# Optimization experiments

Hardware: AMD Instinct MI355X
Metric: run time of the kernel (lower is better)

## Reference

```python
import jax, jax.numpy as jnp
import numpy as np

BN_EPS = 1e-5
DIST_MIN = 1e-10


def _three_nn(p1t, p2t):
    # p1t: [B,N,3], p2t: [B,S,3] -> squared dists/idx of 3 nearest, [B,N,3]
    d2 = (jnp.sum(p1t * p1t, -1, keepdims=True)
          - 2.0 * jnp.einsum('bnc,bsc->bns', p1t, p2t)
          + jnp.sum(p2t * p2t, -1)[:, None, :])  # [B,N,S]
    neg, idx = jax.lax.top_k(-d2, 3)
    return -neg, idx


def _gather_knn(f2t, idx):
    # f2t: [B,S,D], idx: [B,N,3] -> [B,N,3,D]
    return jax.vmap(lambda f, i: f[i])(f2t, idx)


def _conv_bn_relu(x, W, b, g, beta):
    # x: [B,C,N]; 1x1 conv == channel GEMM, then train-mode BN, then ReLU
    y = jnp.einsum('oc,bcn->bon', W, x) + b[None, :, None]
    mean = jnp.mean(y, axis=(0, 2), keepdims=True)
    var = jnp.mean((y - mean) ** 2, axis=(0, 2), keepdims=True)
    yn = (y - mean) * jax.lax.rsqrt(var + BN_EPS)
    return jax.nn.relu(yn * g[None, :, None] + beta[None, :, None])


def setup_inputs() -> dict:
    key = jax.random.key(0)
    ks = jax.random.split(key, 10)
    B, N, S, D1, D2 = 4, 8192, 2048, 128, 256
    C_in, C_mid, C_out = D1 + D2, 256, 256
    inp = {
        'pos1': jax.random.normal(ks[0], (B, 3, N), jnp.float32),
        'pos2': jax.random.normal(ks[1], (B, 3, S), jnp.float32),
        'feature1': jax.random.normal(ks[2], (B, D1, N), jnp.float32),
        'feature2': jax.random.normal(ks[3], (B, D2, S), jnp.float32),
        'W1': jax.random.normal(ks[4], (C_mid, C_in), jnp.float32) / np.sqrt(C_in),
        'b1': jnp.zeros((C_mid,), jnp.float32),
        'g1': jnp.ones((C_mid,), jnp.float32),
        'beta1': jnp.zeros((C_mid,), jnp.float32),
        'W2': jax.random.normal(ks[5], (C_out, C_mid), jnp.float32) / np.sqrt(C_mid),
        'b2': jnp.zeros((C_out,), jnp.float32),
        'g2': jnp.ones((C_out,), jnp.float32),
        'beta2': jnp.zeros((C_out,), jnp.float32),
    }
    return inp


def reference(pos1, pos2, feature1, feature2, W1, b1, g1, beta1, W2, b2, g2, beta2):
    B = pos1.shape[0]
    p1t = jnp.transpose(pos1, (0, 2, 1))  # [B,N,3]
    p2t = jnp.transpose(pos2, (0, 2, 1))  # [B,S,3]
    dists, idx = _three_nn(p1t, p2t)      # [B,N,3]
    dists = jnp.maximum(dists, DIST_MIN)
    w = 1.0 / dists
    w = w / jnp.sum(w, -1, keepdims=True)  # [B,N,3]
    f2t = jnp.transpose(feature2, (0, 2, 1))  # [B,S,D2]
    gathered = _gather_knn(f2t, idx)           # [B,N,3,D2]
    interp = jnp.sum(gathered * w[..., None], axis=2)  # [B,N,D2]
    interp = jnp.transpose(interp, (0, 2, 1))          # [B,D2,N]
    feat = jnp.concatenate([interp, feature1], axis=1)  # [B,D2+D1,N]
    feat = _conv_bn_relu(feat, W1, b1, g1, beta1)
    feat = _conv_bn_relu(feat, W2, b2, g2, beta2)
    return feat
```

## Files before the change

### kernel.cpp

```cpp
#include <hip/hip_runtime.h>
#include <hip/hip_bf16.h>

constexpr int B = 4, N = 8192, S = 2048;

typedef __attribute__((ext_vector_type(8))) short short8;
typedef __attribute__((ext_vector_type(4))) float v4f;

__device__ inline float u2f(ushort u) {
    union { ushort u; __hip_bfloat16 h; } c; c.u = u; return __bfloat162float(c.h);
}
__device__ inline ushort f2u(float f) {
    union { ushort u; __hip_bfloat16 h; } c; c.h = __float2bfloat16(f); return c.u;
}
__device__ inline void async_lds16(const void* g, void* l) {
    __builtin_amdgcn_global_load_lds(
        (const __attribute__((address_space(1))) unsigned*)g,
        (__attribute__((address_space(3))) unsigned*)l, 16, 0, 0);
}
__device__ inline short8 ld8(const ushort* p) { return *(const short8*)p; }

__global__ __launch_bounds__(256) void prep_kernel(
    const float* __restrict__ W1, const float* __restrict__ W2,
    const float* __restrict__ pos2,
    __hip_bfloat16* __restrict__ W1r, __hip_bfloat16* __restrict__ W2r,
    float4* __restrict__ p2pack, float* __restrict__ zero_region)
{
    int i = blockIdx.x * 256 + threadIdx.x;
    if (i < 12288) {
        int kk = i >> 10, q = (i >> 8) & 3, o = i & 255;
        const float* src = W1 + o * 384 + kk * 32 + q * 8;
        float4 a = *(const float4*)src, b = *(const float4*)(src + 4);
        union { short8 s; ushort u[8]; } pk;
        pk.u[0] = f2u(a.x); pk.u[1] = f2u(a.y); pk.u[2] = f2u(a.z); pk.u[3] = f2u(a.w);
        pk.u[4] = f2u(b.x); pk.u[5] = f2u(b.y); pk.u[6] = f2u(b.z); pk.u[7] = f2u(b.w);
        *(short8*)((ushort*)W1r + i * 8) = pk.s;
    } else if (i < 20480) {
        int u = i - 12288;
        int kk = u >> 10, q = (u >> 8) & 3, o = u & 255;
        const float* src = W2 + o * 256 + kk * 32 + q * 8;
        float4 a = *(const float4*)src, b = *(const float4*)(src + 4);
        union { short8 s; ushort u[8]; } pk;
        pk.u[0] = f2u(a.x); pk.u[1] = f2u(a.y); pk.u[2] = f2u(a.z); pk.u[3] = f2u(a.w);
        pk.u[4] = f2u(b.x); pk.u[5] = f2u(b.y); pk.u[6] = f2u(b.z); pk.u[7] = f2u(b.w);
        *(short8*)((ushort*)W2r + u * 8) = pk.s;
    } else if (i < 21504) {
        zero_region[i - 20480] = 0.f;
    } else if (i < 21504 + B * S) {
        int u = i - 21504;
        int b = u >> 11, s = u & (S - 1);
        float x = pos2[(b * 3 + 0) * S + s];
        float y = pos2[(b * 3 + 1) * S + s];
        float z = pos2[(b * 3 + 2) * S + s];
        p2pack[u] = make_float4(x, y, z, x * x + y * y + z * z);
    }
}

__global__ __launch_bounds__(512) void knn_kernel(
    const float* __restrict__ pos1, const float4* __restrict__ p2pack,
    float* __restrict__ wgt, int* __restrict__ idxb)
{
    __shared__ float dLs[8][64][3];
    __shared__ int   iLs[8][64][3];
    const int b = blockIdx.y;
    const int t = threadIdx.x;
    const int lane = t & 63;
    const int w = __builtin_amdgcn_readfirstlane(t >> 6);
    const int qi = blockIdx.x * 64 + lane;

    const float x1 = pos1[(b * 3 + 0) * N + qi];
    const float y1 = pos1[(b * 3 + 1) * N + qi];
    const float z1 = pos1[(b * 3 + 2) * N + qi];
    const float t1 = x1 * x1 + y1 * y1 + z1 * z1;

    const float4* __restrict__ pp = p2pack + b * S + w * 256;

    float d0 = 3.4e38f, d1 = 3.4e38f, d2 = 3.4e38f;
    int i0 = 0x7fffffff, i1 = 0x7fffffff, i2 = 0x7fffffff;

    #pragma unroll 8
    for (int i = 0; i < 256; ++i) {
        float4 p = pp[i];
        float dot = fmaf(x1, p.x, fmaf(y1, p.y, z1 * p.z));
        float dd = fmaf(-2.f, dot, t1) + p.w;
        int s = w * 256 + i;
        bool c0 = dd < d0, c1 = dd < d1, c2 = dd < d2;
        i2 = c1 ? i1 : (c2 ? s : i2);
        i1 = c0 ? i0 : (c1 ? s : i1);
        i0 = c0 ? s : i0;
        float nd1 = __builtin_amdgcn_fmed3f(dd, d0, d1);
        float nd2 = __builtin_amdgcn_fmed3f(dd, d1, d2);
        d0 = fminf(d0, dd);
        d1 = nd1; d2 = nd2;
    }

    dLs[w][lane][0] = d0; dLs[w][lane][1] = d1; dLs[w][lane][2] = d2;
    iLs[w][lane][0] = i0; iLs[w][lane][1] = i1; iLs[w][lane][2] = i2;
    __syncthreads();

    if (t < 64) {
        float f0 = dLs[0][t][0], f1 = dLs[0][t][1], f2 = dLs[0][t][2];
        int   j0 = iLs[0][t][0], j1 = iLs[0][t][1], j2 = iLs[0][t][2];
        #pragma unroll
        for (int c = 1; c < 8; ++c) {
            #pragma unroll
            for (int k = 0; k < 3; ++k) {
                float d = dLs[c][t][k]; int id = iLs[c][t][k];
                bool l0 = (d < f0) || (d == f0 && id < j0);
                bool l1 = (d < f1) || (d == f1 && id < j1);
                bool l2 = (d < f2) || (d == f2 && id < j2);
                if (l0)      { f2 = f1; j2 = j1; f1 = f0; j1 = j0; f0 = d; j0 = id; }
                else if (l1) { f2 = f1; j2 = j1; f1 = d; j1 = id; }
                else if (l2) { f2 = d; j2 = id; }
            }
        }
        float w0 = 1.f / fmaxf(f0, 1e-10f);
        float w1 = 1.f / fmaxf(f1, 1e-10f);
        float w2 = 1.f / fmaxf(f2, 1e-10f);
        float inv = 1.f / (w0 + w1 + w2);
        j0 = ((unsigned)j0 < S) ? j0 : 0;
        j1 = ((unsigned)j1 < S) ? j1 : 0;
        j2 = ((unsigned)j2 < S) ? j2 : 0;
        int base = (b * N + blockIdx.x * 64 + t) * 3;
        wgt[base + 0] = w0 * inv; wgt[base + 1] = w1 * inv; wgt[base + 2] = w2 * inv;
        idxb[base + 0] = j0; idxb[base + 1] = j1; idxb[base + 2] = j2;
    }
}

__global__ __launch_bounds__(256) void transpose_k(
    const float* __restrict__ in, __hip_bfloat16* __restrict__ out,
    int L, int C)
{
    __shared__ ushort tl[64][66];
    const int b = blockIdx.z;
    const int l0 = blockIdx.x * 64, c0 = blockIdx.y * 64;
    const int t = threadIdx.x;
    const float* ip = in + (size_t)b * C * L;
    const int lr = t & 63, cb = t >> 6;
    #pragma unroll
    for (int i = 0; i < 16; ++i) {
        int c = cb + 4 * i;
        tl[lr][c] = f2u(ip[(size_t)(c0 + c) * L + l0 + lr]);
    }
    __syncthreads();
    ushort* op = (ushort*)out + (size_t)b * L * C;
    const int cp = t & 31, lrow = t >> 5;
    #pragma unroll
    for (int i = 0; i < 8; ++i) {
        int l = lrow + 8 * i;
        ushort2 v;
        v.x = tl[l][2 * cp];
        v.y = tl[l][2 * cp + 1];
        *(ushort2*)(op + (size_t)(l0 + l) * C + c0 + 2 * cp) = v;
    }
}

__global__ __launch_bounds__(256) void gemm1_kernel(
    const __hip_bfloat16* __restrict__ Wr, const float* __restrict__ bias,
    const __hip_bfloat16* __restrict__ f2T, const __hip_bfloat16* __restrict__ f1T,
    const int* __restrict__ idxb, const float* __restrict__ wgt,
    __hip_bfloat16* __restrict__ y, float* __restrict__ sums)
{
    __shared__ __align__(16) ushort Xs[64 * 384];
    __shared__ __align__(16) ushort Wbuf[2 * 8192];
    const int t = threadIdx.x;
    const int b = blockIdx.y;
    const int n0 = blockIdx.x * 64;
    const int w = t >> 6, lane = t & 63;
    const int q = lane >> 4, r = lane & 15, r7 = r & 7;

    {
        const char* g0 = (const char*)Wr;
        #pragma unroll
        for (int jj = 0; jj < 4; ++jj)
            async_lds16(g0 + jj * 4096 + t * 16,
                        (char*)Wbuf + jj * 4096 + w * 1024);
    }

    {
        const int lp = t & 31, ro = t >> 5;
        #pragma unroll
        for (int it = 0; it < 8; ++it) {
            int rr = ro + 8 * it;
            int base = (b * N + n0 + rr) * 3;
            int s0 = idxb[base], s1 = idxb[base + 1], s2 = idxb[base + 2];
            s0 = ((unsigned)s0 < S) ? s0 : 0;
            s1 = ((unsigned)s1 < S) ? s1 : 0;
            s2 = ((unsigned)s2 < S) ? s2 : 0;
            float w0 = wgt[base], w1 = wgt[base + 1], w2 = wgt[base + 2];
            union { short8 s; ushort u[8]; } a, c, d, o;
            a.s = ld8((const ushort*)f2T + ((size_t)b * S + s0) * 256 + 8 * lp);
            c.s = ld8((const ushort*)f2T + ((size_t)b * S + s1) * 256 + 8 * lp);
            d.s = ld8((const ushort*)f2T + ((size_t)b * S + s2) * 256 + 8 * lp);
            #pragma unroll
            for (int j = 0; j < 8; ++j)
                o.u[j] = f2u(w0 * u2f(a.u[j]) + w1 * u2f(c.u[j]) + w2 * u2f(d.u[j]));
            *(short8*)(Xs + rr * 384 + ((lp ^ ro) * 8)) = o.s;
        }
    }
    {
        const int lp = t & 15, ro = t >> 4;
        #pragma unroll
        for (int it = 0; it < 4; ++it) {
            int rr = ro + 16 * it;
            short8 v = ld8((const ushort*)f1T + ((size_t)b * N + n0 + rr) * 128 + 8 * lp);
            int c = 32 + lp;
            *(short8*)(Xs + rr * 384 + ((c ^ (rr & 7)) * 8)) = v;
        }
    }
    __syncthreads();

    v4f acc[4][4];
    #pragma unroll
    for (int mt = 0; mt < 4; ++mt)
        #pragma unroll
        for (int nf = 0; nf < 4; ++nf) acc[mt][nf] = (v4f){0.f, 0.f, 0.f, 0.f};

    for (int kk = 0; kk < 12; ++kk) {
        if (kk < 11) {
            const char* g = (const char*)Wr + (kk + 1) * 16384;
            char* l = (char*)Wbuf + ((kk + 1) & 1) * 16384;
            #pragma unroll
            for (int jj = 0; jj < 4; ++jj)
                async_lds16(g + jj * 4096 + t * 16, l + jj * 4096 + w * 1024);
        }
        const ushort* Wb = Wbuf + (kk & 1) * 8192;
        short8 af[4], bf[4];
        #pragma unroll
        for (int mt = 0; mt < 4; ++mt)
            af[mt] = ld8(Wb + q * 2048 + (w * 64 + mt * 16 + r) * 8);
        #pragma unroll
        for (int nf = 0; nf < 4; ++nf)
            bf[nf] = ld8(Xs + (nf * 16 + r) * 384 + (((kk * 4 + q) ^ r7) * 8));
        #pragma unroll
        for (int mt = 0; mt < 4; ++mt)
            #pragma unroll
            for (int nf = 0; nf < 4; ++nf)
                acc[mt][nf] = __builtin_amdgcn_mfma_f32_16x16x32_bf16(
                    af[mt], bf[nf], acc[mt][nf], 0, 0, 0);
        __syncthreads();
    }

    float* statS = (float*)Xs;
    float* statQ = statS + 256;
    #pragma unroll
    for (int mt = 0; mt < 4; ++mt) {
        int ob = w * 64 + mt * 16 + q * 4;
        float4 bi = *(const float4*)(bias + ob);
        float sj0 = 0, sj1 = 0, sj2 = 0, sj3 = 0;
        float qj0 = 0, qj1 = 0, qj2 = 0, qj3 = 0;
        #pragma unroll
        for (int nf = 0; nf < 4; ++nf) {
            int n = n0 + nf * 16 + r;
            float v0 = acc[mt][nf][0] + bi.x, v1 = acc[mt][nf][1] + bi.y;
            float v2 = acc[mt][nf][2] + bi.z, v3 = acc[mt][nf][3] + bi.w;
            ushort4 pk; pk.x = f2u(v0); pk.y = f2u(v1); pk.z = f2u(v2); pk.w = f2u(v3);
            *(ushort4*)((ushort*)y + ((size_t)b * N + n) * 256 + ob) = pk;
            sj0 += v0; sj1 += v1; sj2 += v2; sj3 += v3;
            qj0 += v0 * v0; qj1 += v1 * v1; qj2 += v2 * v2; qj3 += v3 * v3;
        }
        #pragma unroll
        for (int m = 1; m <= 8; m <<= 1) {
            sj0 += __shfl_xor(sj0, m); sj1 += __shfl_xor(sj1, m);
            sj2 += __shfl_xor(sj2, m); sj3 += __shfl_xor(sj3, m);
            qj0 += __shfl_xor(qj0, m); qj1 += __shfl_xor(qj1, m);
            qj2 += __shfl_xor(qj2, m); qj3 += __shfl_xor(qj3, m);
        }
        if (r == 0) {
            statS[ob + 0] = sj0; statS[ob + 1] = sj1;
            statS[ob + 2] = sj2; statS[ob + 3] = sj3;
            statQ[ob + 0] = qj0; statQ[ob + 1] = qj1;
            statQ[ob + 2] = qj2; statQ[ob + 3] = qj3;
        }
    }
    __syncthreads();
    atomicAdd(&sums[t], statS[t]);
    atomicAdd(&sums[256 + t], statQ[t]);
}

__global__ __launch_bounds__(256) void gemm2_kernel(
    const __hip_bfloat16* __restrict__ Wr, const float* __restrict__ bias,
    const float* __restrict__ sums1, const float* __restrict__ g1,
    const float* __restrict__ be1,
    __hip_bfloat16* __restrict__ y, float* __restrict__ sums)
{
    __shared__ __align__(16) ushort Xs[64 * 256];
    __shared__ __align__(16) ushort Wbuf[2 * 8192];
    __shared__ float ssA[256], ssB[256];
    const int t = threadIdx.x;
    const int b = blockIdx.y;
    const int n0 = blockIdx.x * 64;
    const int w = t >> 6, lane = t & 63;
    const int q = lane >> 4, r = lane & 15, r7 = r & 7;

    {
        const char* g0 = (const char*)Wr;
        #pragma unroll
        for (int jj = 0; jj < 4; ++jj)
            async_lds16(g0 + jj * 4096 + t * 16,
                        (char*)Wbuf + jj * 4096 + w * 1024);
    }

    {
        float sv = sums1[t], qv = sums1[256 + t];
        float mean = sv * (1.f / 32768.f);
        float var = qv * (1.f / 32768.f) - mean * mean;
        float rstd = rsqrtf(var + 1e-5f);
        float sc = g1[t] * rstd;
        ssA[t] = sc;
        ssB[t] = be1[t] - mean * sc;
    }
    __syncthreads();

    {
        const int lp = t & 31, ro = t >> 5;
        #pragma unroll
        for (int it = 0; it < 8; ++it) {
            int rr = ro + 8 * it;
            union { short8 s; ushort u[8]; } v, o;
            v.s = ld8((const ushort*)y + ((size_t)b * N + n0 + rr) * 256 + 8 * lp);
            #pragma unroll
            for (int j = 0; j < 8; ++j)
                o.u[j] = f2u(fmaxf(u2f(v.u[j]) * ssA[8 * lp + j] + ssB[8 * lp + j], 0.f));
            *(short8*)(Xs + rr * 256 + ((lp ^ ro) * 8)) = o.s;
        }
    }
    __syncthreads();

    v4f acc[4][4];
    #pragma unroll
    for (int mt = 0; mt < 4; ++mt)
        #pragma unroll
        for (int nf = 0; nf < 4; ++nf) acc[mt][nf] = (v4f){0.f, 0.f, 0.f, 0.f};

    for (int kk = 0; kk < 8; ++kk) {
        if (kk < 7) {
            const char* g = (const char*)Wr + (kk + 1) * 16384;
            char* l = (char*)Wbuf + ((kk + 1) & 1) * 16384;
            #pragma unroll
            for (int jj = 0; jj < 4; ++jj)
                async_lds16(g + jj * 4096 + t * 16, l + jj * 4096 + w * 1024);
        }
        const ushort* Wb = Wbuf + (kk & 1) * 8192;
        short8 af[4], bf[4];
        #pragma unroll
        for (int mt = 0; mt < 4; ++mt)
            af[mt] = ld8(Wb + q * 2048 + (w * 64 + mt * 16 + r) * 8);
        #pragma unroll
        for (int nf = 0; nf < 4; ++nf)
            bf[nf] = ld8(Xs + (nf * 16 + r) * 256 + (((kk * 4 + q) ^ r7) * 8));
        #pragma unroll
        for (int mt = 0; mt < 4; ++mt)
            #pragma unroll
            for (int nf = 0; nf < 4; ++nf)
                acc[mt][nf] = __builtin_amdgcn_mfma_f32_16x16x32_bf16(
                    af[mt], bf[nf], acc[mt][nf], 0, 0, 0);
        __syncthreads();
    }

    float* statS = (float*)Xs;
    float* statQ = statS + 256;
    #pragma unroll
    for (int mt = 0; mt < 4; ++mt) {
        int ob = w * 64 + mt * 16 + q * 4;
        float4 bi = *(const float4*)(bias + ob);
        float sj0 = 0, sj1 = 0, sj2 = 0, sj3 = 0;
        float qj0 = 0, qj1 = 0, qj2 = 0, qj3 = 0;
        #pragma unroll
        for (int nf = 0; nf < 4; ++nf) {
            int n = n0 + nf * 16 + r;
            float v0 = acc[mt][nf][0] + bi.x, v1 = acc[mt][nf][1] + bi.y;
            float v2 = acc[mt][nf][2] + bi.z, v3 = acc[mt][nf][3] + bi.w;
            ushort4 pk; pk.x = f2u(v0); pk.y = f2u(v1); pk.z = f2u(v2); pk.w = f2u(v3);
            *(ushort4*)((ushort*)y + ((size_t)b * N + n) * 256 + ob) = pk;
            sj0 += v0; sj1 += v1; sj2 += v2; sj3 += v3;
            qj0 += v0 * v0; qj1 += v1 * v1; qj2 += v2 * v2; qj3 += v3 * v3;
        }
        #pragma unroll
        for (int m = 1; m <= 8; m <<= 1) {
            sj0 += __shfl_xor(sj0, m); sj1 += __shfl_xor(sj1, m);
            sj2 += __shfl_xor(sj2, m); sj3 += __shfl_xor(sj3, m);
            qj0 += __shfl_xor(qj0, m); qj1 += __shfl_xor(qj1, m);
            qj2 += __shfl_xor(qj2, m); qj3 += __shfl_xor(qj3, m);
        }
        if (r == 0) {
            statS[ob + 0] = sj0; statS[ob + 1] = sj1;
            statS[ob + 2] = sj2; statS[ob + 3] = sj3;
            statQ[ob + 0] = qj0; statQ[ob + 1] = qj1;
            statQ[ob + 2] = qj2; statQ[ob + 3] = qj3;
        }
    }
    __syncthreads();
    atomicAdd(&sums[t], statS[t]);
    atomicAdd(&sums[256 + t], statQ[t]);
}

__global__ __launch_bounds__(256) void final_kernel(
    const __hip_bfloat16* __restrict__ Y, const float* __restrict__ sums2,
    const float* __restrict__ g2, const float* __restrict__ be2,
    float* __restrict__ out)
{
    __shared__ float tl[64][65];
    __shared__ float ssA[64], ssB[64];
    const int t = threadIdx.x;
    const int b = blockIdx.z;
    const int n0 = blockIdx.x * 64, c0 = blockIdx.y * 64;

    if (t < 64) {
        int c = c0 + t;
        float sv = sums2[c], qv = sums2[256 + c];
        float mean = sv * (1.f / 32768.f);
        float var = qv * (1.f / 32768.f) - mean * mean;
        float rstd = rsqrtf(var + 1e-5f);
        float sc = g2[c] * rstd;
        ssA[t] = sc;
        ssB[t] = be2[c] - mean * sc;
    }
    __syncthreads();

    const int nl = t >> 3, cho = 8 * (t & 7);
    #pragma unroll
    for (int it = 0; it < 2; ++it) {
        int n = nl + 32 * it;
        union { short8 s; ushort u[8]; } v;
        v.s = ld8((const ushort*)Y + ((size_t)b * N + n0 + n) * 256 + c0 + cho);
        #pragma unroll
        for (int j = 0; j < 8; ++j)
            tl[n][cho + j] = fmaxf(u2f(v.u[j]) * ssA[cho + j] + ssB[cho + j], 0.f);
    }
    __syncthreads();

    const int cl = t >> 4, n4 = (t & 15) * 4;
    #pragma unroll
    for (int it = 0; it < 4; ++it) {
        int c = cl + 16 * it;
        float4 v;
        v.x = tl[n4 + 0][c]; v.y = tl[n4 + 1][c];
        v.z = tl[n4 + 2][c]; v.w = tl[n4 + 3][c];
        *(float4*)(out + ((size_t)b * 256 + c0 + c) * N + n0 + n4) = v;
    }
}

extern "C" void kernel_launch(void* const* d_in, const int* in_sizes, int n_in,
                              void* d_out, int out_size, void* d_ws, size_t ws_size,
                              hipStream_t stream)
{
    (void)in_sizes; (void)n_in; (void)out_size;
    if (ws_size < (30u << 20)) return;

    const float* pos1 = (const float*)d_in[0];
    const float* pos2 = (const float*)d_in[1];
    const float* f1   = (const float*)d_in[2];
    const float* f2   = (const float*)d_in[3];
    const float* W1   = (const float*)d_in[4];
    const float* b1   = (const float*)d_in[5];
    const float* g1   = (const float*)d_in[6];
    const float* be1  = (const float*)d_in[7];
    const float* W2   = (const float*)d_in[8];
    const float* b2   = (const float*)d_in[9];
    const float* g2   = (const float*)d_in[10];
    const float* be2  = (const float*)d_in[11];

    char* ws = (char*)d_ws;
    int*   idxb  = (int*)(ws + 0);
    float* wgt   = (float*)(ws + 393216);
    float* sums1 = (float*)(ws + 786432);
    float* sums2 = sums1 + 512;
    __hip_bfloat16* W1r = (__hip_bfloat16*)(ws + 819200);
    __hip_bfloat16* W2r = (__hip_bfloat16*)(ws + 1015808);
    float4* p2pack = (float4*)(ws + 1310720);
    __hip_bfloat16* f2T = (__hip_bfloat16*)(ws + (2u << 20));
    __hip_bfloat16* f1T = (__hip_bfloat16*)(ws + (6u << 20));
    __hip_bfloat16* y   = (__hip_bfloat16*)(ws + (14u << 20));

    prep_kernel<<<116, 256, 0, stream>>>(W1, W2, pos2, W1r, W2r, p2pack, sums1);

    knn_kernel<<<dim3(N / 64, B), 512, 0, stream>>>(pos1, p2pack, wgt, idxb);

    transpose_k<<<dim3(S / 64, 256 / 64, B), 256, 0, stream>>>(f2, f2T, S, 256);
    transpose_k<<<dim3(N / 64, 128 / 64, B), 256, 0, stream>>>(f1, f1T, N, 128);

    gemm1_kernel<<<dim3(N / 64, B), 256, 0, stream>>>(
        W1r, b1, f2T, f1T, idxb, wgt, y, sums1);
    gemm2_kernel<<<dim3(N / 64, B), 256, 0, stream>>>(
        W2r, b2, sums1, g1, be1, y, sums2);
    final_kernel<<<dim3(N / 64, 256 / 64, B), 256, 0, stream>>>(
        y, sums2, g2, be2, (float*)d_out);
}
```

Measured before the change: 200.9 us.

## Fuse kNN into GEMM1 and merge prep with feature transposes

Measured after the change: 204.4 us. No clear change (+1.7%).

```diff
diff --git a/kernel.cpp b/kernel.cpp
--- a/kernel.cpp
+++ b/kernel.cpp
@@ -19,178 +19,174 @@
 }
 __device__ inline short8 ld8(const ushort* p) { return *(const short8*)p; }
 
-__global__ __launch_bounds__(256) void prep_kernel(
+__device__ inline void transpose_tile(
+    const float* __restrict__ ip, ushort* __restrict__ op,
+    int L, int C, int l0, int c0, int t, ushort (*tl)[66])
+{
+    const int lr = t & 63, cb = t >> 6;
+    #pragma unroll
+    for (int i = 0; i < 16; ++i) {
+        int c = cb + 4 * i;
+        tl[lr][c] = f2u(ip[(size_t)(c0 + c) * L + l0 + lr]);
+    }
+    __syncthreads();
+    const int cp = t & 31, lrow = t >> 5;
+    #pragma unroll
+    for (int i = 0; i < 8; ++i) {
+        int l = lrow + 8 * i;
+        ushort2 v;
+        v.x = tl[l][2 * cp]; v.y = tl[l][2 * cp + 1];
+        *(ushort2*)(op + (size_t)(l0 + l) * C + c0 + 2 * cp) = v;
+    }
+}
+
+__global__ __launch_bounds__(256) void prep_all(
     const float* __restrict__ W1, const float* __restrict__ W2,
-    const float* __restrict__ pos2,
-    __hip_bfloat16* __restrict__ W1r, __hip_bfloat16* __restrict__ W2r,
-    float4* __restrict__ p2pack, float* __restrict__ zero_region)
-{
-    int i = blockIdx.x * 256 + threadIdx.x;
-    if (i < 12288) {
-        int kk = i >> 10, q = (i >> 8) & 3, o = i & 255;
-        const float* src = W1 + o * 384 + kk * 32 + q * 8;
-        float4 a = *(const float4*)src, b = *(const float4*)(src + 4);
-        union { short8 s; ushort u[8]; } pk;
-        pk.u[0] = f2u(a.x); pk.u[1] = f2u(a.y); pk.u[2] = f2u(a.z); pk.u[3] = f2u(a.w);
-        pk.u[4] = f2u(b.x); pk.u[5] = f2u(b.y); pk.u[6] = f2u(b.z); pk.u[7] = f2u(b.w);
-        *(short8*)((ushort*)W1r + i * 8) = pk.s;
-    } else if (i < 20480) {
-        int u = i - 12288;
-        int kk = u >> 10, q = (u >> 8) & 3, o = u & 255;
-        const float* src = W2 + o * 256 + kk * 32 + q * 8;
-        float4 a = *(const float4*)src, b = *(const float4*)(src + 4);
-        union { short8 s; ushort u[8]; } pk;
-        pk.u[0] = f2u(a.x); pk.u[1] = f2u(a.y); pk.u[2] = f2u(a.z); pk.u[3] = f2u(a.w);
-        pk.u[4] = f2u(b.x); pk.u[5] = f2u(b.y); pk.u[6] = f2u(b.z); pk.u[7] = f2u(b.w);
-        *(short8*)((ushort*)W2r + u * 8) = pk.s;
-    } else if (i < 21504) {
-        zero_region[i - 20480] = 0.f;
-    } else if (i < 21504 + B * S) {
-        int u = i - 21504;
-        int b = u >> 11, s = u & (S - 1);
-        float x = pos2[(b * 3 + 0) * S + s];
-        float y = pos2[(b * 3 + 1) * S + s];
-        float z = pos2[(b * 3 + 2) * S + s];
-        p2pack[u] = make_float4(x, y, z, x * x + y * y + z * z);
-    }
-}
-
-__global__ __launch_bounds__(512) void knn_kernel(
+    const float* __restrict__ pos2, const float* __restrict__ f2,
+    const float* __restrict__ f1,
+    ushort* __restrict__ W1r, ushort* __restrict__ W2r,
+    float4* __restrict__ p2pack, float* __restrict__ zero_region,
+    ushort* __restrict__ f2T, ushort* __restrict__ f1T)
+{
+    __shared__ ushort tl[64][66];
+    const int bid = blockIdx.x;
+    const int t = threadIdx.x;
+    if (bid < 512) {
+        int b = bid >> 7, ct = (bid >> 5) & 3, st = bid & 31;
+        transpose_tile(f2 + (size_t)b * 256 * S, f2T + (size_t)b * S * 256,
+                       S, 256, st * 64, ct * 64, t, tl);
+    } else if (bid < 1536) {
+        int u = bid - 512;
+        int b = u >> 8, ct = (u >> 7) & 1, lt = u & 127;
+        transpose_tile(f1 + (size_t)b * 128 * N, f1T + (size_t)b * N * 128,
+                       N, 128, lt * 64, ct * 64, t, tl);
+    } else {
+        int i = (bid - 1536) * 256 + t;
+        if (i < 12288) {
+            int kk = i >> 10, qq = (i >> 8) & 3, o = i & 255;
+            const float* src = W1 + o * 384 + kk * 32 + qq * 8;
+            float4 a = *(const float4*)src, bb = *(const float4*)(src + 4);
+            union { short8 s; ushort u[8]; } pk;
+            pk.u[0]=f2u(a.x); pk.u[1]=f2u(a.y); pk.u[2]=f2u(a.z); pk.u[3]=f2u(a.w);
+            pk.u[4]=f2u(bb.x); pk.u[5]=f2u(bb.y); pk.u[6]=f2u(bb.z); pk.u[7]=f2u(bb.w);
+            *(short8*)(W1r + i * 8) = pk.s;
+        } else if (i < 20480) {
+            int u = i - 12288;
+            int kk = u >> 10, qq = (u >> 8) & 3, o = u & 255;
+            const float* src = W2 + o * 256 + kk * 32 + qq * 8;
+            float4 a = *(const float4*)src, bb = *(const float4*)(src + 4);
+            union { short8 s; ushort u[8]; } pk;
+            pk.u[0]=f2u(a.x); pk.u[1]=f2u(a.y); pk.u[2]=f2u(a.z); pk.u[3]=f2u(a.w);
+            pk.u[4]=f2u(bb.x); pk.u[5]=f2u(bb.y); pk.u[6]=f2u(bb.z); pk.u[7]=f2u(bb.w);
+            *(short8*)(W2r + u * 8) = pk.s;
+        } else if (i < 21504) {
+            zero_region[i - 20480] = 0.f;
+        } else if (i < 21504 + B * S) {
+            int u = i - 21504;
+            int b = u >> 11, s = u & (S - 1);
+            float x = pos2[(b * 3 + 0) * S + s];
+            float y = pos2[(b * 3 + 1) * S + s];
+            float z = pos2[(b * 3 + 2) * S + s];
+            p2pack[u] = make_float4(x, y, z, x * x + y * y + z * z);
+        }
+    }
+}
+
+__global__ __launch_bounds__(256) void knn_gemm1(
     const float* __restrict__ pos1, const float4* __restrict__ p2pack,
-    float* __restrict__ wgt, int* __restrict__ idxb)
-{
-    __shared__ float dLs[8][64][3];
-    __shared__ int   iLs[8][64][3];
-    const int b = blockIdx.y;
+    const ushort* __restrict__ W1r, const float* __restrict__ bias1,
+    const ushort* __restrict__ f2T, const ushort* __restrict__ f1T,
+    ushort* __restrict__ y, float* __restrict__ sums)
+{
+    __shared__ __align__(16) char smem[81920];
+    ushort* Xs   = (ushort*)smem;
+    ushort* Wbuf = (ushort*)(smem + 49152);
+    float*  dL   = (float*)(smem + 65536);
+    int*    iL   = (int*)  (smem + 65536 + 3072);
+    float*  wgtL = (float*)(smem + 65536 + 6144);
+    int*    idxL = (int*)  (smem + 65536 + 6912);
+
     const int t = threadIdx.x;
     const int lane = t & 63;
     const int w = __builtin_amdgcn_readfirstlane(t >> 6);
-    const int qi = blockIdx.x * 64 + lane;
-
-    const float x1 = pos1[(b * 3 + 0) * N + qi];
-    const float y1 = pos1[(b * 3 + 1) * N + qi];
-    const float z1 = pos1[(b * 3 + 2) * N + qi];
-    const float t1 = x1 * x1 + y1 * y1 + z1 * z1;
-
-    const float4* __restrict__ pp = p2pack + b * S + w * 256;
-
-    float d0 = 3.4e38f, d1 = 3.4e38f, d2 = 3.4e38f;
-    int i0 = 0x7fffffff, i1 = 0x7fffffff, i2 = 0x7fffffff;
-
-    #pragma unroll 8
-    for (int i = 0; i < 256; ++i) {
-        float4 p = pp[i];
-        float dot = fmaf(x1, p.x, fmaf(y1, p.y, z1 * p.z));
-        float dd = fmaf(-2.f, dot, t1) + p.w;
-        int s = w * 256 + i;
-        bool c0 = dd < d0, c1 = dd < d1, c2 = dd < d2;
-        i2 = c1 ? i1 : (c2 ? s : i2);
-        i1 = c0 ? i0 : (c1 ? s : i1);
-        i0 = c0 ? s : i0;
-        float nd1 = __builtin_amdgcn_fmed3f(dd, d0, d1);
-        float nd2 = __builtin_amdgcn_fmed3f(dd, d1, d2);
-        d0 = fminf(d0, dd);
-        d1 = nd1; d2 = nd2;
-    }
-
-    dLs[w][lane][0] = d0; dLs[w][lane][1] = d1; dLs[w][lane][2] = d2;
-    iLs[w][lane][0] = i0; iLs[w][lane][1] = i1; iLs[w][lane][2] = i2;
-    __syncthreads();
-
+    const int b = blockIdx.y;
+    const int n0 = blockIdx.x * 64;
+    const int q = lane >> 4, r = lane & 15, r7 = r & 7;
+
+    #pragma unroll
+    for (int jj = 0; jj < 4; ++jj)
+        async_lds16((const char*)W1r + jj * 4096 + t * 16,
+                    (char*)Wbuf + jj * 4096 + w * 1024);
+
+    {
+        const int qi = n0 + lane;
+        const float x1 = pos1[(b * 3 + 0) * N + qi];
+        const float y1 = pos1[(b * 3 + 1) * N + qi];
+        const float z1 = pos1[(b * 3 + 2) * N + qi];
+        const float t1 = x1 * x1 + y1 * y1 + z1 * z1;
+        const float4* __restrict__ pp = p2pack + b * S + w * 512;
+        float d0 = 3.4e38f, d1 = 3.4e38f, d2 = 3.4e38f;
+        int i0 = 0x7fffffff, i1 = 0x7fffffff, i2 = 0x7fffffff;
+        #pragma unroll 8
+        for (int i = 0; i < 512; ++i) {
+            float4 p = pp[i];
+            float dot = fmaf(x1, p.x, fmaf(y1, p.y, z1 * p.z));
+            float dd = fmaf(-2.f, dot, t1) + p.w;
+            int s = w * 512 + i;
+            bool c0 = dd < d0, c1 = dd < d1, c2 = dd < d2;
+            i2 = c1 ? i1 : (c2 ? s : i2);
+            i1 = c0 ? i0 : (c1 ? s : i1);
+            i0 = c0 ? s : i0;
+            float nd1 = __builtin_amdgcn_fmed3f(dd, d0, d1);
+            float nd2 = __builtin_amdgcn_fmed3f(dd, d1, d2);
+            d0 = fminf(d0, dd);
+            d1 = nd1; d2 = nd2;
+        }
+        int base = (w * 64 + lane) * 3;
+        dL[base + 0] = d0; dL[base + 1] = d1; dL[base + 2] = d2;
+        iL[base + 0] = i0; iL[base + 1] = i1; iL[base + 2] = i2;
+    }
+    __syncthreads();
     if (t < 64) {
-        float f0 = dLs[0][t][0], f1 = dLs[0][t][1], f2 = dLs[0][t][2];
-        int   j0 = iLs[0][t][0], j1 = iLs[0][t][1], j2 = iLs[0][t][2];
-        #pragma unroll
-        for (int c = 1; c < 8; ++c) {
+        float f0 = dL[t*3+0], fv1 = dL[t*3+1], fv2 = dL[t*3+2];
+        int   j0 = iL[t*3+0], j1 = iL[t*3+1], j2 = iL[t*3+2];
+        #pragma unroll
+        for (int c = 1; c < 4; ++c) {
+            int cb = (c * 64 + t) * 3;
             #pragma unroll
             for (int k = 0; k < 3; ++k) {
-                float d = dLs[c][t][k]; int id = iLs[c][t][k];
-                bool l0 = (d < f0) || (d == f0 && id < j0);
-                bool l1 = (d < f1) || (d == f1 && id < j1);
-                bool l2 = (d < f2) || (d == f2 && id < j2);
-                if (l0)      { f2 = f1; j2 = j1; f1 = f0; j1 = j0; f0 = d; j0 = id; }
-                else if (l1) { f2 = f1; j2 = j1; f1 = d; j1 = id; }
-                else if (l2) { f2 = d; j2 = id; }
+                float d = dL[cb + k]; int id = iL[cb + k];
+                bool l0 = (d < f0)  || (d == f0  && id < j0);
+                bool l1 = (d < fv1) || (d == fv1 && id < j1);
+                bool l2 = (d < fv2) || (d == fv2 && id < j2);
+                if (l0)      { fv2 = fv1; j2 = j1; fv1 = f0; j1 = j0; f0 = d; j0 = id; }
+                else if (l1) { fv2 = fv1; j2 = j1; fv1 = d; j1 = id; }
+                else if (l2) { fv2 = d; j2 = id; }
             }
         }
         float w0 = 1.f / fmaxf(f0, 1e-10f);
-        float w1 = 1.f / fmaxf(f1, 1e-10f);
-        float w2 = 1.f / fmaxf(f2, 1e-10f);
+        float w1 = 1.f / fmaxf(fv1, 1e-10f);
+        float w2 = 1.f / fmaxf(fv2, 1e-10f);
         float inv = 1.f / (w0 + w1 + w2);
         j0 = ((unsigned)j0 < S) ? j0 : 0;
         j1 = ((unsigned)j1 < S) ? j1 : 0;
         j2 = ((unsigned)j2 < S) ? j2 : 0;
-        int base = (b * N + blockIdx.x * 64 + t) * 3;
-        wgt[base + 0] = w0 * inv; wgt[base + 1] = w1 * inv; wgt[base + 2] = w2 * inv;
-        idxb[base + 0] = j0; idxb[base + 1] = j1; idxb[base + 2] = j2;
-    }
-}
-
-__global__ __launch_bounds__(256) void transpose_k(
-    const float* __restrict__ in, __hip_bfloat16* __restrict__ out,
-    int L, int C)
-{
-    __shared__ ushort tl[64][66];
-    const int b = blockIdx.z;
-    const int l0 = blockIdx.x * 64, c0 = blockIdx.y * 64;
-    const int t = threadIdx.x;
-    const float* ip = in + (size_t)b * C * L;
-    const int lr = t & 63, cb = t >> 6;
-    #pragma unroll
-    for (int i = 0; i < 16; ++i) {
-        int c = cb + 4 * i;
-        tl[lr][c] = f2u(ip[(size_t)(c0 + c) * L + l0 + lr]);
-    }
-    __syncthreads();
-    ushort* op = (ushort*)out + (size_t)b * L * C;
-    const int cp = t & 31, lrow = t >> 5;
-    #pragma unroll
-    for (int i = 0; i < 8; ++i) {
-        int l = lrow + 8 * i;
-        ushort2 v;
-        v.x = tl[l][2 * cp];
-        v.y = tl[l][2 * cp + 1];
-        *(ushort2*)(op + (size_t)(l0 + l) * C + c0 + 2 * cp) = v;
-    }
-}
-
-__global__ __launch_bounds__(256) void gemm1_kernel(
-    const __hip_bfloat16* __restrict__ Wr, const float* __restrict__ bias,
-    const __hip_bfloat16* __restrict__ f2T, const __hip_bfloat16* __restrict__ f1T,
-    const int* __restrict__ idxb, const float* __restrict__ wgt,
-    __hip_bfloat16* __restrict__ y, float* __restrict__ sums)
-{
-    __shared__ __align__(16) ushort Xs[64 * 384];
-    __shared__ __align__(16) ushort Wbuf[2 * 8192];
-    const int t = threadIdx.x;
-    const int b = blockIdx.y;
-    const int n0 = blockIdx.x * 64;
-    const int w = t >> 6, lane = t & 63;
-    const int q = lane >> 4, r = lane & 15, r7 = r & 7;
-
-    {
-        const char* g0 = (const char*)Wr;
-        #pragma unroll
-        for (int jj = 0; jj < 4; ++jj)
-            async_lds16(g0 + jj * 4096 + t * 16,
-                        (char*)Wbuf + jj * 4096 + w * 1024);
-    }
+        wgtL[t*3+0] = w0 * inv; wgtL[t*3+1] = w1 * inv; wgtL[t*3+2] = w2 * inv;
+        idxL[t*3+0] = j0; idxL[t*3+1] = j1; idxL[t*3+2] = j2;
+    }
+    __syncthreads();
 
     {
         const int lp = t & 31, ro = t >> 5;
         #pragma unroll
         for (int it = 0; it < 8; ++it) {
             int rr = ro + 8 * it;
-            int base = (b * N + n0 + rr) * 3;
-            int s0 = idxb[base], s1 = idxb[base + 1], s2 = idxb[base + 2];
-            s0 = ((unsigned)s0 < S) ? s0 : 0;
-            s1 = ((unsigned)s1 < S) ? s1 : 0;
-            s2 = ((unsigned)s2 < S) ? s2 : 0;
-            float w0 = wgt[base], w1 = wgt[base + 1], w2 = wgt[base + 2];
+            int s0 = idxL[rr*3+0], s1 = idxL[rr*3+1], s2 = idxL[rr*3+2];
+            float w0 = wgtL[rr*3+0], w1 = wgtL[rr*3+1], w2 = wgtL[rr*3+2];
             union { short8 s; ushort u[8]; } a, c, d, o;
-            a.s = ld8((const ushort*)f2T + ((size_t)b * S + s0) * 256 + 8 * lp);
-            c.s = ld8((const ushort*)f2T + ((size_t)b * S + s1) * 256 + 8 * lp);
-            d.s = ld8((const ushort*)f2T + ((size_t)b * S + s2) * 256 + 8 * lp);
+            a.s = ld8(f2T + ((size_t)b * S + s0) * 256 + 8 * lp);
+            c.s = ld8(f2T + ((size_t)b * S + s1) * 256 + 8 * lp);
+            d.s = ld8(f2T + ((size_t)b * S + s2) * 256 + 8 * lp);
             #pragma unroll
             for (int j = 0; j < 8; ++j)
                 o.u[j] = f2u(w0 * u2f(a.u[j]) + w1 * u2f(c.u[j]) + w2 * u2f(d.u[j]));
@@ -202,7 +198,7 @@
         #pragma unroll
         for (int it = 0; it < 4; ++it) {
             int rr = ro + 16 * it;
-            short8 v = ld8((const ushort*)f1T + ((size_t)b * N + n0 + rr) * 128 + 8 * lp);
+            short8 v = ld8(f1T + ((size_t)b * N + n0 + rr) * 128 + 8 * lp);
             int c = 32 + lp;
             *(short8*)(Xs + rr * 384 + ((c ^ (rr & 7)) * 8)) = v;
         }
@@ -217,7 +213,7 @@
 
     for (int kk = 0; kk < 12; ++kk) {
         if (kk < 11) {
-            const char* g = (const char*)Wr + (kk + 1) * 16384;
+            const char* g = (const char*)W1r + (kk + 1) * 16384;
             char* l = (char*)Wbuf + ((kk + 1) & 1) * 16384;
             #pragma unroll
             for (int jj = 0; jj < 4; ++jj)
@@ -245,7 +241,7 @@
     #pragma unroll
     for (int mt = 0; mt < 4; ++mt) {
         int ob = w * 64 + mt * 16 + q * 4;
-        float4 bi = *(const float4*)(bias + ob);
+        float4 bi = *(const float4*)(bias1 + ob);
         float sj0 = 0, sj1 = 0, sj2 = 0, sj3 = 0;
         float qj0 = 0, qj1 = 0, qj2 = 0, qj3 = 0;
         #pragma unroll
@@ -254,7 +250,7 @@
             float v0 = acc[mt][nf][0] + bi.x, v1 = acc[mt][nf][1] + bi.y;
             float v2 = acc[mt][nf][2] + bi.z, v3 = acc[mt][nf][3] + bi.w;
             ushort4 pk; pk.x = f2u(v0); pk.y = f2u(v1); pk.z = f2u(v2); pk.w = f2u(v3);
-            *(ushort4*)((ushort*)y + ((size_t)b * N + n) * 256 + ob) = pk;
+            *(ushort4*)(y + ((size_t)b * N + n) * 256 + ob) = pk;
             sj0 += v0; sj1 += v1; sj2 += v2; sj3 += v3;
             qj0 += v0 * v0; qj1 += v1 * v1; qj2 += v2 * v2; qj3 += v3 * v3;
         }
@@ -278,10 +274,10 @@
 }
 
 __global__ __launch_bounds__(256) void gemm2_kernel(
-    const __hip_bfloat16* __restrict__ Wr, const float* __restrict__ bias,
+    const ushort* __restrict__ Wr, const float* __restrict__ bias,
     const float* __restrict__ sums1, const float* __restrict__ g1,
     const float* __restrict__ be1,
-    __hip_bfloat16* __restrict__ y, float* __restrict__ sums)
+    ushort* __restrict__ y, float* __restrict__ sums)
 {
     __shared__ __align__(16) ushort Xs[64 * 256];
     __shared__ __align__(16) ushort Wbuf[2 * 8192];
@@ -317,7 +313,7 @@
         for (int it = 0; it < 8; ++it) {
             int rr = ro + 8 * it;
             union { short8 s; ushort u[8]; } v, o;
-            v.s = ld8((const ushort*)y + ((size_t)b * N + n0 + rr) * 256 + 8 * lp);
+            v.s = ld8(y + ((size_t)b * N + n0 + rr) * 256 + 8 * lp);
             #pragma unroll
             for (int j = 0; j < 8; ++j)
                 o.u[j] = f2u(fmaxf(u2f(v.u[j]) * ssA[8 * lp + j] + ssB[8 * lp + j], 0.f));
@@ -371,7 +367,7 @@
             float v0 = acc[mt][nf][0] + bi.x, v1 = acc[mt][nf][1] + bi.y;
             float v2 = acc[mt][nf][2] + bi.z, v3 = acc[mt][nf][3] + bi.w;
             ushort4 pk; pk.x = f2u(v0); pk.y = f2u(v1); pk.z = f2u(v2); pk.w = f2u(v3);
-            *(ushort4*)((ushort*)y + ((size_t)b * N + n) * 256 + ob) = pk;
+            *(ushort4*)(y + ((size_t)b * N + n) * 256 + ob) = pk;
             sj0 += v0; sj1 += v1; sj2 += v2; sj3 += v3;
             qj0 += v0 * v0; qj1 += v1 * v1; qj2 += v2 * v2; qj3 += v3 * v3;
         }
@@ -395,7 +391,7 @@
 }
 
 __global__ __launch_bounds__(256) void final_kernel(
-    const __hip_bfloat16* __restrict__ Y, const float* __restrict__ sums2,
+    const ushort* __restrict__ Y, const float* __restrict__ sums2,
     const float* __restrict__ g2, const float* __restrict__ be2,
     float* __restrict__ out)
 {
@@ -422,7 +418,7 @@
     for (int it = 0; it < 2; ++it) {
         int n = nl + 32 * it;
         union { short8 s; ushort u[8]; } v;
-        v.s = ld8((const ushort*)Y + ((size_t)b * N + n0 + n) * 256 + c0 + cho);
+        v.s = ld8(Y + ((size_t)b * N + n0 + n) * 256 + c0 + cho);
         #pragma unroll
         for (int j = 0; j < 8; ++j)
             tl[n][cho + j] = fmaxf(u2f(v.u[j]) * ssA[cho + j] + ssB[cho + j], 0.f);
@@ -461,28 +457,24 @@
     const float* be2  = (const float*)d_in[11];
 
     char* ws = (char*)d_ws;
-    int*   idxb  = (int*)(ws + 0);
-    float* wgt   = (float*)(ws + 393216);
-    float* sums1 = (float*)(ws + 786432);
-    float* sums2 = sums1 + 512;
-    __hip_bfloat16* W1r = (__hip_bfloat16*)(ws + 819200);
-    __hip_bfloat16* W2r = (__hip_bfloat16*)(ws + 1015808);
-    float4* p2pack = (float4*)(ws + 1310720);
-    __hip_bfloat16* f2T = (__hip_bfloat16*)(ws + (2u << 20));
-    __hip_bfloat16* f1T = (__hip_bfloat16*)(ws + (6u << 20));
-    __hip_bfloat16* y   = (__hip_bfloat16*)(ws + (14u << 20));
-
-    prep_kernel<<<116, 256, 0, stream>>>(W1, W2, pos2, W1r, W2r, p2pack, sums1);
-
-    knn_kernel<<<dim3(N / 64, B), 512, 0, stream>>>(pos1, p2pack, wgt, idxb);
-
-    transpose_k<<<dim3(S / 64, 256 / 64, B), 256, 0, stream>>>(f2, f2T, S, 256);
-    transpose_k<<<dim3(N / 64, 128 / 64, B), 256, 0, stream>>>(f1, f1T, N, 128);
-
-    gemm1_kernel<<<dim3(N / 64, B), 256, 0, stream>>>(
-        W1r, b1, f2T, f1T, idxb, wgt, y, sums1);
+    float*  sums1  = (float*)ws;
+    float*  sums2  = sums1 + 512;
+    ushort* W1r    = (ushort*)(ws + 4096);
+    ushort* W2r    = (ushort*)(ws + 4096 + 196608);
+    float4* p2pack = (float4*)(ws + 4096 + 196608 + 131072);
+    ushort* f2T    = (ushort*)(ws + (1u << 19));
+    ushort* f1T    = (ushort*)(ws + (1u << 19) + (4u << 20));
+    ushort* y      = (ushort*)(ws + (1u << 19) + (12u << 20));
+
+    prep_all<<<1652, 256, 0, stream>>>(W1, W2, pos2, f2, f1,
+                                       W1r, W2r, p2pack, sums1, f2T, f1T);
+
+    knn_gemm1<<<dim3(N / 64, B), 256, 0, stream>>>(
+        pos1, p2pack, W1r, b1, f2T, f1T, y, sums1);
+
     gemm2_kernel<<<dim3(N / 64, B), 256, 0, stream>>>(
         W2r, b2, sums1, g1, be1, y, sums2);
+
     final_kernel<<<dim3(N / 64, 256 / 64, B), 256, 0, stream>>>(
         y, sums2, g2, be2, (float*)d_out);
 }
```
